# Kernel optimization log

Hardware: AMD Instinct MI355X
Metric: run time of the kernel (lower is better)

Reference implementation:

```python
import jax, jax.numpy as jnp
import numpy as np

HIDDEN = 64


def _lstm_cell(x, h, c, W_ih, W_hh, b_ih, b_hh):
    # gates: [B, 4*H], torch LSTMCell order: i, f, g, o
    gates = x @ W_ih.T + h @ W_hh.T + b_ih + b_hh
    i, f, g, o = jnp.split(gates, 4, axis=-1)
    i = jax.nn.sigmoid(i)
    f = jax.nn.sigmoid(f)
    g = jnp.tanh(g)
    o = jax.nn.sigmoid(o)
    c_new = f * c + i * g
    h_new = o * jnp.tanh(c_new)
    return h_new, c_new


def setup_inputs() -> dict:
    key = jax.random.key(0)
    ks = jax.random.split(key, 12)
    B, L, H = 1024, 512, HIDDEN
    k = 1.0 / np.sqrt(H)  # torch LSTMCell/Linear init scale
    u = lambda kk, shape: jax.random.uniform(kk, shape, jnp.float32, -k, k)
    return {
        "y": jax.random.normal(ks[0], (B, L), jnp.float32),
        "W_ih1": u(ks[1], (4 * H, 1)),
        "W_hh1": u(ks[2], (4 * H, H)),
        "b_ih1": u(ks[3], (4 * H,)),
        "b_hh1": u(ks[4], (4 * H,)),
        "W_ih2": u(ks[5], (4 * H, H)),
        "W_hh2": u(ks[6], (4 * H, H)),
        "b_ih2": u(ks[7], (4 * H,)),
        "b_hh2": u(ks[8], (4 * H,)),
        "W_lin": u(ks[9], (1, H)),
        "b_lin": u(ks[10], (1,)),
        "future_preds": 0,
    }


def reference(y, W_ih1, W_hh1, b_ih1, b_hh1, W_ih2, W_hh2, b_ih2, b_hh2,
              W_lin, b_lin, future_preds):
    B = y.shape[0]
    H = HIDDEN
    zeros = jnp.zeros((B, H), jnp.float32)

    def step(carry, x_t):
        h1, c1, h2, c2 = carry
        h1, c1 = _lstm_cell(x_t, h1, c1, W_ih1, W_hh1, b_ih1, b_hh1)
        h2, c2 = _lstm_cell(h1, h2, c2, W_ih2, W_hh2, b_ih2, b_hh2)
        out = h2 @ W_lin.T + b_lin  # [B, 1]
        return (h1, c1, h2, c2), out

    xs = y.T[:, :, None]  # [L, B, 1]
    carry, outs = jax.lax.scan(step, (zeros, zeros, zeros, zeros), xs)
    outputs = outs[:, :, 0].T  # [B, L]

    if future_preds > 0:
        def fstep(fc, _):
            h1, c1, h2, c2, out = fc
            h1, c1 = _lstm_cell(out, h1, c1, W_ih1, W_hh1, b_ih1, b_hh1)
            h2, c2 = _lstm_cell(h1, h2, c2, W_ih2, W_hh2, b_ih2, b_hh2)
            out = h2 @ W_lin.T + b_lin
            return (h1, c1, h2, c2, out), out
        last_out = outs[-1]  # [B, 1]
        _, fouts = jax.lax.scan(fstep, (*carry, last_out), None,
                                length=future_preds)
        outputs = jnp.concatenate([outputs, fouts[:, :, 0].T], axis=1)
    return outputs
```

## Files before the change

### kernel.cpp

```cpp
#include <hip/hip_runtime.h>
#include <math.h>

#define LSEQ 512

typedef float  f32x4  __attribute__((ext_vector_type(4)));
typedef short  bf16x8 __attribute__((ext_vector_type(8)));

union Frag { uint32_t u[4]; bf16x8 h; };

__device__ __forceinline__ float frcp(float x)  { return __builtin_amdgcn_rcpf(x); }
__device__ __forceinline__ float fexp2(float x) { return __builtin_amdgcn_exp2f(x); }

__device__ __forceinline__ f32x4 vexp2(f32x4 x) {
    f32x4 r;
    r.x = fexp2(x.x); r.y = fexp2(x.y); r.z = fexp2(x.z); r.w = fexp2(x.w);
    return r;
}
__device__ __forceinline__ f32x4 vrcp(f32x4 x) {
    f32x4 r;
    r.x = frcp(x.x); r.y = frcp(x.y); r.z = frcp(x.z); r.w = frcp(x.w);
    return r;
}
__device__ __forceinline__ f32x4 vsigm(f32x4 x) {
    f32x4 e = vexp2(x * -1.442695041f);
    return vrcp(e + 1.0f);
}
__device__ __forceinline__ f32x4 vtanh(f32x4 x) {
    f32x4 e = vexp2(x * 2.885390082f);
    return 1.0f - 2.0f * vrcp(e + 1.0f);
}

__device__ __forceinline__ uint32_t pack_hi_u(uint32_t b0, uint32_t b1) {
    return __builtin_amdgcn_perm(b1, b0, 0x07060302u);
}

__device__ __forceinline__ void load_wfrag(const float* __restrict__ W, int sl, int nn, int g4,
                                           Frag fh[4][2], Frag fl[4][2]) {
#pragma unroll
    for (int gt = 0; gt < 4; ++gt) {
        const float* p = W + (size_t)(64 * gt + 16 * sl + nn) * 64 + g4 * 8;
#pragma unroll
        for (int kt = 0; kt < 2; ++kt) {
            float4 va = ((const float4*)(p + kt * 32))[0];
            float4 vb = ((const float4*)(p + kt * 32))[1];
            float v[8] = {va.x, va.y, va.z, va.w, vb.x, vb.y, vb.z, vb.w};
#pragma unroll
            for (int j = 0; j < 4; ++j) {
                uint32_t b0 = __float_as_uint(v[2 * j]);
                uint32_t b1 = __float_as_uint(v[2 * j + 1]);
                float l0 = v[2 * j]     - __uint_as_float(b0 & 0xffff0000u);
                float l1 = v[2 * j + 1] - __uint_as_float(b1 & 0xffff0000u);
                fh[gt][kt].u[j] = pack_hi_u(b0, b1);
                fl[gt][kt].u[j] = pack_hi_u(__float_as_uint(l0), __float_as_uint(l1));
            }
        }
    }
}

__device__ __forceinline__ int hidx(int m, int j) {
    return m * 64 + ((((j >> 3) ^ (m & 7)) << 3) | (j & 7));
}

__device__ __forceinline__ void loadA(const uint16_t* __restrict__ ph,
                                      const uint16_t* __restrict__ pl,
                                      int mm, int g4, bf16x8 ah[2], bf16x8 al[2]) {
#pragma unroll
    for (int kt = 0; kt < 2; ++kt) {
        const int off = mm * 64 + ((((kt << 2) + g4) ^ (mm & 7)) << 3);
        ah[kt] = *(const bf16x8*)(ph + off);
        al[kt] = *(const bf16x8*)(pl + off);
    }
}

__device__ __forceinline__ void split_store(uint16_t* ph, uint16_t* pl, int idx, float x) {
    uint32_t xb = __float_as_uint(x);
    ph[idx] = (uint16_t)(xb >> 16);
    float lo = x - __uint_as_float(xb & 0xffff0000u);
    pl[idx] = (uint16_t)(__float_as_uint(lo) >> 16);
}

#define MFMA3(acc, AH, AL, BH, BL)                                                  \
    acc = __builtin_amdgcn_mfma_f32_16x16x32_bf16((AH), (BH).h, acc, 0, 0, 0);      \
    acc = __builtin_amdgcn_mfma_f32_16x16x32_bf16((AH), (BL).h, acc, 0, 0, 0);      \
    acc = __builtin_amdgcn_mfma_f32_16x16x32_bf16((AL), (BH).h, acc, 0, 0, 0);

__global__ __launch_bounds__(512, 1)
void lstm2_pipe(const float* __restrict__ y,
                const float* __restrict__ W_ih1, const float* __restrict__ W_hh1,
                const float* __restrict__ b_ih1, const float* __restrict__ b_hh1,
                const float* __restrict__ W_ih2, const float* __restrict__ W_hh2,
                const float* __restrict__ b_ih2, const float* __restrict__ b_hh2,
                const float* __restrict__ W_lin, const float* __restrict__ b_lin,
                float* __restrict__ out)
{
    __shared__ __align__(16) float    y_s[LSEQ * 16];
    __shared__ __align__(16) uint16_t h1h[2][1024];
    __shared__ __align__(16) uint16_t h1l[2][1024];
    __shared__ __align__(16) uint16_t h2h[2][1024];
    __shared__ __align__(16) uint16_t h2l[2][1024];
    __shared__ __align__(16) float    outS[16 * 521];

    const int tid  = threadIdx.x;
    const int w    = tid >> 6;
    const int lane = tid & 63;
    const int nn   = lane & 15;
    const int g4   = lane >> 4;
    const int mq   = g4 << 2;
    const int bg0  = blockIdx.x << 4;

    {
        const int m = tid >> 5, seg = tid & 31;
        const float4* yp = (const float4*)(y + (size_t)(bg0 + m) * LSEQ) + seg * 4;
#pragma unroll
        for (int c = 0; c < 4; ++c) {
            float4 v = yp[c];
            int t0 = seg * 16 + c * 4;
            y_s[(t0 + 0) * 16 + m] = v.x;
            y_s[(t0 + 1) * 16 + m] = v.y;
            y_s[(t0 + 2) * 16 + m] = v.z;
            y_s[(t0 + 3) * 16 + m] = v.w;
        }
        if (tid < 256) {
            uint4 z = {0u, 0u, 0u, 0u};
            ((uint4*)h1h)[tid] = z;
            ((uint4*)h1l)[tid] = z;
            ((uint4*)h2h)[tid] = z;
            ((uint4*)h2l)[tid] = z;
        }
    }
    __syncthreads();

    if (w < 4) {
        Frag bh[4][2], bl[4][2];
        load_wfrag(W_hh1, w, nn, g4, bh, bl);
        float bs1_[4], wih1_[4];
#pragma unroll
        for (int gt = 0; gt < 4; ++gt) {
            int row = 64 * gt + 16 * w + nn;
            bs1_[gt]  = b_ih1[row] + b_hh1[row];
            wih1_[gt] = W_ih1[row];
        }
        const int jj = 16 * w + nn;
        f32x4 c1v = {0.f, 0.f, 0.f, 0.f};

        float wl[16];
        const float blin = b_lin[0];
        {
            const float4* wp = (const float4*)W_lin + g4 * 4;
#pragma unroll
            for (int i = 0; i < 4; ++i) {
                float4 v = wp[i];
                wl[4 * i + 0] = v.x; wl[4 * i + 1] = v.y;
                wl[4 * i + 2] = v.z; wl[4 * i + 3] = v.w;
            }
        }

#pragma unroll 1
        for (int t = 0; t <= LSEQ; ++t) {
            if (t < LSEQ) {
                bf16x8 ah[2], al[2];
                loadA(h1h[(t + 1) & 1], h1l[(t + 1) & 1], nn, g4, ah, al);
                f32x4 xq = *(const f32x4*)&y_s[t * 16 + mq];
                f32x4 ac0[4], ac1[4];
#pragma unroll
                for (int g = 0; g < 4; ++g) {
                    ac0[g] = xq * wih1_[g] + bs1_[g];
                    ac1[g] = 0.f;
                }
                __builtin_amdgcn_s_setprio(1);
#pragma unroll
                for (int g = 0; g < 4; ++g) {
                    MFMA3(ac0[g], ah[0], al[0], bh[g][0], bl[g][0]);
                    MFMA3(ac1[g], ah[1], al[1], bh[g][1], bl[g][1]);
                }
                __builtin_amdgcn_s_setprio(0);
                f32x4 gi = vsigm(ac0[0] + ac1[0]);
                f32x4 gf = vsigm(ac0[1] + ac1[1]);
                f32x4 gg = vtanh(ac0[2] + ac1[2]);
                f32x4 go = vsigm(ac0[3] + ac1[3]);
                c1v = gf * c1v + gi * gg;
                f32x4 h1v = go * vtanh(c1v);
#pragma unroll
                for (int r = 0; r < 4; ++r)
                    split_store(h1h[t & 1], h1l[t & 1], hidx(mq + r, jj), h1v[r]);
            }
            if (t >= 2 && w == ((t - 2) & 3)) {
                const uint16_t* ph = h2h[t & 1];
                const uint16_t* pl = h2l[t & 1];
                const int m = lane & 15;
                float s = 0.f;
#pragma unroll
                for (int oo = 0; oo < 2; ++oo) {
                    const int oct = 2 * g4 + oo;
                    const int off = m * 64 + ((oct ^ (m & 7)) << 3);
                    bf16x8 hv = *(const bf16x8*)(ph + off);
                    bf16x8 lv = *(const bf16x8*)(pl + off);
#pragma unroll
                    for (int i = 0; i < 8; ++i) {
                        float val = __uint_as_float(((uint32_t)(uint16_t)hv[i]) << 16)
                                  + __uint_as_float(((uint32_t)(uint16_t)lv[i]) << 16);
                        s = fmaf(val, wl[oo * 8 + i], s);
                    }
                }
                s += __shfl_xor(s, 16);
                s += __shfl_xor(s, 32);
                if (lane < 16) outS[m * 521 + (t - 2)] = s + blin;
            }
            __syncthreads();
        }
        if (w == 0) {
            const uint16_t* ph = h2h[1];
            const uint16_t* pl = h2l[1];
            const int m = lane & 15;
            float s = 0.f;
#pragma unroll
            for (int oo = 0; oo < 2; ++oo) {
                const int oct = 2 * g4 + oo;
                const int off = m * 64 + ((oct ^ (m & 7)) << 3);
                bf16x8 hv = *(const bf16x8*)(ph + off);
                bf16x8 lv = *(const bf16x8*)(pl + off);
#pragma unroll
                for (int i = 0; i < 8; ++i) {
                    float val = __uint_as_float(((uint32_t)(uint16_t)hv[i]) << 16)
                              + __uint_as_float(((uint32_t)(uint16_t)lv[i]) << 16);
                    s = fmaf(val, wl[oo * 8 + i], s);
                }
            }
            s += __shfl_xor(s, 16);
            s += __shfl_xor(s, 32);
            if (lane < 16) outS[m * 521 + (LSEQ - 1)] = s + blin;
        }
    } else {
        const int v = w - 4;
        Frag bih[4][2], bil[4][2], bhh[4][2], bhl[4][2];
        load_wfrag(W_ih2, v, nn, g4, bih, bil);
        load_wfrag(W_hh2, v, nn, g4, bhh, bhl);
        float bs2_[4];
#pragma unroll
        for (int gt = 0; gt < 4; ++gt) {
            int row = 64 * gt + 16 * v + nn;
            bs2_[gt] = b_ih2[row] + b_hh2[row];
        }
        const int jj = 16 * v + nn;
        f32x4 c2v = {0.f, 0.f, 0.f, 0.f};

#pragma unroll 1
        for (int t = 0; t <= LSEQ; ++t) {
            if (t >= 1) {
                bf16x8 a3h_[2], a3l_[2], a2h_[2], a2l_[2];
                loadA(h2h[t & 1],       h2l[t & 1],       nn, g4, a3h_, a3l_);
                loadA(h1h[(t - 1) & 1], h1l[(t - 1) & 1], nn, g4, a2h_, a2l_);
                f32x4 aca[4], acb[4];
#pragma unroll
                for (int g = 0; g < 4; ++g) { acb[g] = bs2_[g]; aca[g] = 0.f; }
                __builtin_amdgcn_s_setprio(1);
#pragma unroll
                for (int kt = 0; kt < 2; ++kt)
#pragma unroll
                    for (int g = 0; g < 4; ++g) {
                        MFMA3(acb[g], a3h_[kt], a3l_[kt], bhh[g][kt], bhl[g][kt]);
                        MFMA3(aca[g], a2h_[kt], a2l_[kt], bih[g][kt], bil[g][kt]);
                    }
                __builtin_amdgcn_s_setprio(0);
                f32x4 gi = vsigm(aca[0] + acb[0]);
                f32x4 gf = vsigm(aca[1] + acb[1]);
                f32x4 gg = vtanh(aca[2] + acb[2]);
                f32x4 go = vsigm(aca[3] + acb[3]);
                c2v = gf * c2v + gi * gg;
                f32x4 h2v = go * vtanh(c2v);
#pragma unroll
                for (int r = 0; r < 4; ++r)
                    split_store(h2h[(t - 1) & 1], h2l[(t - 1) & 1], hidx(mq + r, jj), h2v[r]);
            }
            __syncthreads();
        }
    }

    __syncthreads();

    {
        const int m  = tid >> 5;
        const int t0 = (tid & 31) << 4;
        float* op = out + (size_t)(bg0 + m) * LSEQ + t0;
        const float* sp = outS + m * 521 + t0;
#pragma unroll
        for (int k2 = 0; k2 < 4; ++k2) {
            float4 vv = make_float4(sp[4 * k2 + 0], sp[4 * k2 + 1],
                                    sp[4 * k2 + 2], sp[4 * k2 + 3]);
            *(float4*)(op + 4 * k2) = vv;
        }
    }
}

extern "C" void kernel_launch(void* const* d_in, const int* in_sizes, int n_in,
                              void* d_out, int out_size, void* d_ws, size_t ws_size,
                              hipStream_t stream) {
    const float* y     = (const float*)d_in[0];
    const float* W_ih1 = (const float*)d_in[1];
    const float* W_hh1 = (const float*)d_in[2];
    const float* b_ih1 = (const float*)d_in[3];
    const float* b_hh1 = (const float*)d_in[4];
    const float* W_ih2 = (const float*)d_in[5];
    const float* W_hh2 = (const float*)d_in[6];
    const float* b_ih2 = (const float*)d_in[7];
    const float* b_hh2 = (const float*)d_in[8];
    const float* W_lin = (const float*)d_in[9];
    const float* b_lin = (const float*)d_in[10];
    float* out = (float*)d_out;

    lstm2_pipe<<<dim3(64), dim3(512), 0, stream>>>(
        y, W_ih1, W_hh1, b_ih1, b_hh1, W_ih2, W_hh2, b_ih2, b_hh2,
        W_lin, b_lin, out);
}
```

Baseline: 678.1 us.

## Rebalance MFMA work by offloading half of layer-2 input projection to layer-1 warps

Layer-1 warps now also compute the first K-half of the layer-2 input projection (W_ih2 · h1) and pass partial gate sums to layer-2 warps through a double-buffered shared array. Layer-2 warps then do only the second K-half plus the recurrent matmul. This evens out the MFMA count per step between the two warp groups. It also spreads the output dot product across all 8 warps. The cost is a deeper pipeline (h1 buffers widened to 4 slots, two extra steps), extra LDS traffic for the partial sums, and more shared memory use.

After: 714.3 us. 5.3% more time.

```diff
diff --git a/kernel.cpp b/kernel.cpp
--- a/kernel.cpp
+++ b/kernel.cpp
@@ -57,6 +57,26 @@
     }
 }
 
+__device__ __forceinline__ void load_wfrag_kt(const float* __restrict__ W, int sl, int nn,
+                                              int g4, int kt, Frag fh[4], Frag fl[4]) {
+#pragma unroll
+    for (int gt = 0; gt < 4; ++gt) {
+        const float* p = W + (size_t)(64 * gt + 16 * sl + nn) * 64 + g4 * 8 + kt * 32;
+        float4 va = ((const float4*)p)[0];
+        float4 vb = ((const float4*)p)[1];
+        float v[8] = {va.x, va.y, va.z, va.w, vb.x, vb.y, vb.z, vb.w};
+#pragma unroll
+        for (int j = 0; j < 4; ++j) {
+            uint32_t b0 = __float_as_uint(v[2 * j]);
+            uint32_t b1 = __float_as_uint(v[2 * j + 1]);
+            float l0 = v[2 * j]     - __uint_as_float(b0 & 0xffff0000u);
+            float l1 = v[2 * j + 1] - __uint_as_float(b1 & 0xffff0000u);
+            fh[gt].u[j] = pack_hi_u(b0, b1);
+            fl[gt].u[j] = pack_hi_u(__float_as_uint(l0), __float_as_uint(l1));
+        }
+    }
+}
+
 __device__ __forceinline__ int hidx(int m, int j) {
     return m * 64 + ((((j >> 3) ^ (m & 7)) << 3) | (j & 7));
 }
@@ -83,6 +103,30 @@
     acc = __builtin_amdgcn_mfma_f32_16x16x32_bf16((AH), (BH).h, acc, 0, 0, 0);      \
     acc = __builtin_amdgcn_mfma_f32_16x16x32_bf16((AH), (BL).h, acc, 0, 0, 0);      \
     acc = __builtin_amdgcn_mfma_f32_16x16x32_bf16((AL), (BH).h, acc, 0, 0, 0);
+
+__device__ __forceinline__ void out_dot(const uint16_t* __restrict__ ph,
+                                        const uint16_t* __restrict__ pl,
+                                        int lane, int g4, const float* wl, float blin,
+                                        float* __restrict__ outS, int tprime) {
+    const int m = lane & 15;
+    float s = 0.f;
+#pragma unroll
+    for (int oo = 0; oo < 2; ++oo) {
+        const int oct = 2 * g4 + oo;
+        const int off = m * 64 + ((oct ^ (m & 7)) << 3);
+        bf16x8 hv = *(const bf16x8*)(ph + off);
+        bf16x8 lv = *(const bf16x8*)(pl + off);
+#pragma unroll
+        for (int i = 0; i < 8; ++i) {
+            float val = __uint_as_float(((uint32_t)(uint16_t)hv[i]) << 16)
+                      + __uint_as_float(((uint32_t)(uint16_t)lv[i]) << 16);
+            s = fmaf(val, wl[oo * 8 + i], s);
+        }
+    }
+    s += __shfl_xor(s, 16);
+    s += __shfl_xor(s, 32);
+    if (lane < 16) outS[m * 521 + tprime] = s + blin;
+}
 
 __global__ __launch_bounds__(512, 1)
 void lstm2_pipe(const float* __restrict__ y,
@@ -94,10 +138,11 @@
                 float* __restrict__ out)
 {
     __shared__ __align__(16) float    y_s[LSEQ * 16];
-    __shared__ __align__(16) uint16_t h1h[2][1024];
-    __shared__ __align__(16) uint16_t h1l[2][1024];
+    __shared__ __align__(16) uint16_t h1h[4][1024];
+    __shared__ __align__(16) uint16_t h1l[4][1024];
     __shared__ __align__(16) uint16_t h2h[2][1024];
     __shared__ __align__(16) uint16_t h2l[2][1024];
+    __shared__ __align__(16) float    ihAs[2 * 4 * 4 * 256];
     __shared__ __align__(16) float    outS[16 * 521];
 
     const int tid  = threadIdx.x;
@@ -120,158 +165,132 @@
             y_s[(t0 + 2) * 16 + m] = v.z;
             y_s[(t0 + 3) * 16 + m] = v.w;
         }
+        uint4 z = {0u, 0u, 0u, 0u};
+        ((uint4*)h1h)[tid] = z;
+        ((uint4*)h1l)[tid] = z;
         if (tid < 256) {
-            uint4 z = {0u, 0u, 0u, 0u};
-            ((uint4*)h1h)[tid] = z;
-            ((uint4*)h1l)[tid] = z;
             ((uint4*)h2h)[tid] = z;
             ((uint4*)h2l)[tid] = z;
         }
     }
     __syncthreads();
+
+    float wl[16];
+    const float blin = b_lin[0];
+    {
+        const float4* wp = (const float4*)W_lin + g4 * 4;
+#pragma unroll
+        for (int i = 0; i < 4; ++i) {
+            float4 v = wp[i];
+            wl[4 * i + 0] = v.x; wl[4 * i + 1] = v.y;
+            wl[4 * i + 2] = v.z; wl[4 * i + 3] = v.w;
+        }
+    }
 
     if (w < 4) {
         Frag bh[4][2], bl[4][2];
         load_wfrag(W_hh1, w, nn, g4, bh, bl);
-        float bs1_[4], wih1_[4];
+        Frag bi0h_[4], bi0l_[4];
+        load_wfrag_kt(W_ih2, w, nn, g4, 0, bi0h_, bi0l_);
+        float bs1_[4], wih1_[4], bs2_[4];
 #pragma unroll
         for (int gt = 0; gt < 4; ++gt) {
             int row = 64 * gt + 16 * w + nn;
             bs1_[gt]  = b_ih1[row] + b_hh1[row];
             wih1_[gt] = W_ih1[row];
+            bs2_[gt]  = b_ih2[row] + b_hh2[row];
         }
         const int jj = 16 * w + nn;
         f32x4 c1v = {0.f, 0.f, 0.f, 0.f};
 
-        float wl[16];
-        const float blin = b_lin[0];
-        {
-            const float4* wp = (const float4*)W_lin + g4 * 4;
-#pragma unroll
-            for (int i = 0; i < 4; ++i) {
-                float4 v = wp[i];
-                wl[4 * i + 0] = v.x; wl[4 * i + 1] = v.y;
-                wl[4 * i + 2] = v.z; wl[4 * i + 3] = v.w;
+#pragma unroll 1
+        for (int t = 0; t <= LSEQ + 2; ++t) {
+            if (t <= LSEQ) {
+                bf16x8 ah[2], al[2];
+                loadA(h1h[(t + 3) & 3], h1l[(t + 3) & 3], nn, g4, ah, al);
+                f32x4 ai[4];
+#pragma unroll
+                for (int g = 0; g < 4; ++g) ai[g] = bs2_[g];
+                if (t < LSEQ) {
+                    f32x4 xq = *(const f32x4*)&y_s[t * 16 + mq];
+                    f32x4 ac[4];
+#pragma unroll
+                    for (int g = 0; g < 4; ++g) ac[g] = xq * wih1_[g] + bs1_[g];
+                    __builtin_amdgcn_s_setprio(1);
+#pragma unroll
+                    for (int g = 0; g < 4; ++g) {
+                        MFMA3(ac[g], ah[0], al[0], bh[g][0], bl[g][0]);
+                        MFMA3(ac[g], ah[1], al[1], bh[g][1], bl[g][1]);
+                    }
+#pragma unroll
+                    for (int g = 0; g < 4; ++g) {
+                        MFMA3(ai[g], ah[0], al[0], bi0h_[g], bi0l_[g]);
+                    }
+                    __builtin_amdgcn_s_setprio(0);
+                    f32x4 gi = vsigm(ac[0]);
+                    f32x4 gf = vsigm(ac[1]);
+                    f32x4 gg = vtanh(ac[2]);
+                    f32x4 go = vsigm(ac[3]);
+                    c1v = gf * c1v + gi * gg;
+                    f32x4 h1v = go * vtanh(c1v);
+#pragma unroll
+                    for (int r = 0; r < 4; ++r)
+                        split_store(h1h[t & 3], h1l[t & 3], hidx(mq + r, jj), h1v[r]);
+                } else {
+#pragma unroll
+                    for (int g = 0; g < 4; ++g) {
+                        MFMA3(ai[g], ah[0], al[0], bi0h_[g], bi0l_[g]);
+                    }
+                }
+                float* ip = &ihAs[((t & 1) * 4 + w) * 4 * 256 + (lane << 2)];
+#pragma unroll
+                for (int g = 0; g < 4; ++g) *(f32x4*)(ip + g * 256) = ai[g];
             }
-        }
+            if (t >= 3 && w == ((t - 3) & 7))
+                out_dot(h2h[(t + 1) & 1], h2l[(t + 1) & 1], lane, g4, wl, blin, outS, t - 3);
+            __syncthreads();
+        }
+    } else {
+        const int v = w - 4;
+        Frag bhh_[4][2], bhl_[4][2];
+        load_wfrag(W_hh2, v, nn, g4, bhh_, bhl_);
+        Frag bi1h_[4], bi1l_[4];
+        load_wfrag_kt(W_ih2, v, nn, g4, 1, bi1h_, bi1l_);
+        const int jj = 16 * v + nn;
+        f32x4 c2v = {0.f, 0.f, 0.f, 0.f};
 
 #pragma unroll 1
-        for (int t = 0; t <= LSEQ; ++t) {
-            if (t < LSEQ) {
-                bf16x8 ah[2], al[2];
-                loadA(h1h[(t + 1) & 1], h1l[(t + 1) & 1], nn, g4, ah, al);
-                f32x4 xq = *(const f32x4*)&y_s[t * 16 + mq];
-                f32x4 ac0[4], ac1[4];
+        for (int t = 0; t <= LSEQ + 2; ++t) {
+            if (t >= 2 && t <= LSEQ + 1) {
+                bf16x8 a3h_[2], a3l_[2];
+                loadA(h2h[(t + 1) & 1], h2l[(t + 1) & 1], nn, g4, a3h_, a3l_);
+                const int off1 = nn * 64 + (((4 + g4) ^ (nn & 7)) << 3);
+                bf16x8 a2h1 = *(const bf16x8*)(&h1h[(t + 2) & 3][0] + off1);
+                bf16x8 a2l1 = *(const bf16x8*)(&h1l[(t + 2) & 3][0] + off1);
+                const float* ip = &ihAs[(((t - 1) & 1) * 4 + v) * 4 * 256 + (lane << 2)];
+                f32x4 acc[4];
+#pragma unroll
+                for (int g = 0; g < 4; ++g) acc[g] = *(const f32x4*)(ip + g * 256);
+                __builtin_amdgcn_s_setprio(1);
 #pragma unroll
                 for (int g = 0; g < 4; ++g) {
-                    ac0[g] = xq * wih1_[g] + bs1_[g];
-                    ac1[g] = 0.f;
-                }
-                __builtin_amdgcn_s_setprio(1);
-#pragma unroll
-                for (int g = 0; g < 4; ++g) {
-                    MFMA3(ac0[g], ah[0], al[0], bh[g][0], bl[g][0]);
-                    MFMA3(ac1[g], ah[1], al[1], bh[g][1], bl[g][1]);
+                    MFMA3(acc[g], a2h1, a2l1, bi1h_[g], bi1l_[g]);
+                    MFMA3(acc[g], a3h_[0], a3l_[0], bhh_[g][0], bhl_[g][0]);
+                    MFMA3(acc[g], a3h_[1], a3l_[1], bhh_[g][1], bhl_[g][1]);
                 }
                 __builtin_amdgcn_s_setprio(0);
-                f32x4 gi = vsigm(ac0[0] + ac1[0]);
-                f32x4 gf = vsigm(ac0[1] + ac1[1]);
-                f32x4 gg = vtanh(ac0[2] + ac1[2]);
-                f32x4 go = vsigm(ac0[3] + ac1[3]);
-                c1v = gf * c1v + gi * gg;
-                f32x4 h1v = go * vtanh(c1v);
-#pragma unroll
-                for (int r = 0; r < 4; ++r)
-                    split_store(h1h[t & 1], h1l[t & 1], hidx(mq + r, jj), h1v[r]);
-            }
-            if (t >= 2 && w == ((t - 2) & 3)) {
-                const uint16_t* ph = h2h[t & 1];
-                const uint16_t* pl = h2l[t & 1];
-                const int m = lane & 15;
-                float s = 0.f;
-#pragma unroll
-                for (int oo = 0; oo < 2; ++oo) {
-                    const int oct = 2 * g4 + oo;
-                    const int off = m * 64 + ((oct ^ (m & 7)) << 3);
-                    bf16x8 hv = *(const bf16x8*)(ph + off);
-                    bf16x8 lv = *(const bf16x8*)(pl + off);
-#pragma unroll
-                    for (int i = 0; i < 8; ++i) {
-                        float val = __uint_as_float(((uint32_t)(uint16_t)hv[i]) << 16)
-                                  + __uint_as_float(((uint32_t)(uint16_t)lv[i]) << 16);
-                        s = fmaf(val, wl[oo * 8 + i], s);
-                    }
-                }
-                s += __shfl_xor(s, 16);
-                s += __shfl_xor(s, 32);
-                if (lane < 16) outS[m * 521 + (t - 2)] = s + blin;
-            }
-            __syncthreads();
-        }
-        if (w == 0) {
-            const uint16_t* ph = h2h[1];
-            const uint16_t* pl = h2l[1];
-            const int m = lane & 15;
-            float s = 0.f;
-#pragma unroll
-            for (int oo = 0; oo < 2; ++oo) {
-                const int oct = 2 * g4 + oo;
-                const int off = m * 64 + ((oct ^ (m & 7)) << 3);
-                bf16x8 hv = *(const bf16x8*)(ph + off);
-                bf16x8 lv = *(const bf16x8*)(pl + off);
-#pragma unroll
-                for (int i = 0; i < 8; ++i) {
-                    float val = __uint_as_float(((uint32_t)(uint16_t)hv[i]) << 16)
-                              + __uint_as_float(((uint32_t)(uint16_t)lv[i]) << 16);
-                    s = fmaf(val, wl[oo * 8 + i], s);
-                }
-            }
-            s += __shfl_xor(s, 16);
-            s += __shfl_xor(s, 32);
-            if (lane < 16) outS[m * 521 + (LSEQ - 1)] = s + blin;
-        }
-    } else {
-        const int v = w - 4;
-        Frag bih[4][2], bil[4][2], bhh[4][2], bhl[4][2];
-        load_wfrag(W_ih2, v, nn, g4, bih, bil);
-        load_wfrag(W_hh2, v, nn, g4, bhh, bhl);
-        float bs2_[4];
-#pragma unroll
-        for (int gt = 0; gt < 4; ++gt) {
-            int row = 64 * gt + 16 * v + nn;
-            bs2_[gt] = b_ih2[row] + b_hh2[row];
-        }
-        const int jj = 16 * v + nn;
-        f32x4 c2v = {0.f, 0.f, 0.f, 0.f};
-
-#pragma unroll 1
-        for (int t = 0; t <= LSEQ; ++t) {
-            if (t >= 1) {
-                bf16x8 a3h_[2], a3l_[2], a2h_[2], a2l_[2];
-                loadA(h2h[t & 1],       h2l[t & 1],       nn, g4, a3h_, a3l_);
-                loadA(h1h[(t - 1) & 1], h1l[(t - 1) & 1], nn, g4, a2h_, a2l_);
-                f32x4 aca[4], acb[4];
-#pragma unroll
-                for (int g = 0; g < 4; ++g) { acb[g] = bs2_[g]; aca[g] = 0.f; }
-                __builtin_amdgcn_s_setprio(1);
-#pragma unroll
-                for (int kt = 0; kt < 2; ++kt)
-#pragma unroll
-                    for (int g = 0; g < 4; ++g) {
-                        MFMA3(acb[g], a3h_[kt], a3l_[kt], bhh[g][kt], bhl[g][kt]);
-                        MFMA3(aca[g], a2h_[kt], a2l_[kt], bih[g][kt], bil[g][kt]);
-                    }
-                __builtin_amdgcn_s_setprio(0);
-                f32x4 gi = vsigm(aca[0] + acb[0]);
-                f32x4 gf = vsigm(aca[1] + acb[1]);
-                f32x4 gg = vtanh(aca[2] + acb[2]);
-                f32x4 go = vsigm(aca[3] + acb[3]);
+                f32x4 gi = vsigm(acc[0]);
+                f32x4 gf = vsigm(acc[1]);
+                f32x4 gg = vtanh(acc[2]);
+                f32x4 go = vsigm(acc[3]);
                 c2v = gf * c2v + gi * gg;
                 f32x4 h2v = go * vtanh(c2v);
 #pragma unroll
                 for (int r = 0; r < 4; ++r)
-                    split_store(h2h[(t - 1) & 1], h2l[(t - 1) & 1], hidx(mq + r, jj), h2v[r]);
+                    split_store(h2h[t & 1], h2l[t & 1], hidx(mq + r, jj), h2v[r]);
             }
+            if (t >= 3 && w == ((t - 3) & 7))
+                out_dot(h2h[(t + 1) & 1], h2l[(t + 1) & 1], lane, g4, wl, blin, outS, t - 3);
             __syncthreads();
         }
     }
```
